# Performance work log

Measured on AMD Instinct MI355X. Metric: run time of the kernel, lower is better.

The kernel has to match this reference:

```python
import jax, jax.numpy as jnp
import numpy as np
from jax import lax

D = 33            # n_vertices
NEG_SLOPE = 0.2   # LeakyReLU slope
EPS_IN = 1e-5     # InstanceNorm eps


def _block(x, w, b, gamma, beta):
    # Conv2d(k=3, stride=2, pad=1) -> LeakyReLU(0.2) -> optional InstanceNorm2d(affine)
    y = lax.conv_general_dilated(x, w, (2, 2), [(1, 1), (1, 1)],
                                 dimension_numbers=('NCHW', 'OIHW', 'NCHW'))
    y = y + b[None, :, None, None]
    y = jnp.where(y >= 0, y, NEG_SLOPE * y)
    if gamma is not None:
        mu = jnp.mean(y, (2, 3), keepdims=True)
        var = jnp.var(y, (2, 3), keepdims=True)
        y = (y - mu) * lax.rsqrt(var + EPS_IN) * gamma[None, :, None, None] + beta[None, :, None, None]
    return y


def _backbone(lq, w1, b1, g1, be1, w2, b2, g2, be2, w3, b3, g3, be3,
              w4, b4, g4, be4, w5, b5):
    B = lq.shape[0]
    # F.interpolate(..., 256, bilinear, align_corners=False) == half-pixel linear, no antialias
    x = jax.image.resize(lq, (B, 3, 256, 256), method='linear', antialias=False)
    x = _block(x, w1, b1, g1, be1)   # [B,16,128,128]
    x = _block(x, w2, b2, g2, be2)   # [B,32,64,64]
    x = _block(x, w3, b3, g3, be3)   # [B,64,32,32]
    x = _block(x, w4, b4, g4, be4)   # [B,128,16,16]
    x = _block(x, w5, b5, None, None)  # [B,128,8,8]; Dropout is identity in eval
    # AdaptiveAvgPool2d(2) on 8x8 -> mean over 4x4 blocks
    x = x.reshape(B, 128, 2, 4, 2, 4).mean((3, 5))  # [B,128,2,2]
    return x.reshape(B, -1)  # [B,512]


def _trilerp(lut, r, g, b):
    # lut [3,D,D,D]; r,g,b [N] in [0, D-1]; align_corners=True + border padding
    i0 = jnp.clip(jnp.floor(r).astype(jnp.int32), 0, D - 2)
    j0 = jnp.clip(jnp.floor(g).astype(jnp.int32), 0, D - 2)
    k0 = jnp.clip(jnp.floor(b).astype(jnp.int32), 0, D - 2)
    fr, fg, fb = r - i0, g - j0, b - k0

    def c(di, dj, dk):
        return lut[:, i0 + di, j0 + dj, k0 + dk]  # [3,N]

    return (c(0, 0, 0) * (1 - fr) * (1 - fg) * (1 - fb)
            + c(0, 0, 1) * (1 - fr) * (1 - fg) * fb
            + c(0, 1, 0) * (1 - fr) * fg * (1 - fb)
            + c(0, 1, 1) * (1 - fr) * fg * fb
            + c(1, 0, 0) * fr * (1 - fg) * (1 - fb)
            + c(1, 0, 1) * fr * (1 - fg) * fb
            + c(1, 1, 0) * fr * fg * (1 - fb)
            + c(1, 1, 1) * fr * fg * fb)


def _ailut_transform(img, luts, vertices):
    # img [B,3,H,W] in [0,1]; luts [B,3,D,D,D]; vertices [B,3,D] sorted in [0,1]
    B, C, H, W = img.shape
    p = img.reshape(B, C, -1)  # [B,3,N]
    # per-(b,c) searchsorted(right=True)
    idx = jax.vmap(jax.vmap(lambda v, x: jnp.searchsorted(v, x, side='right')))(vertices, p)
    idx = jnp.clip(idx, 1, D - 1)
    v_lo = jnp.take_along_axis(vertices, idx - 1, axis=-1)
    v_hi = jnp.take_along_axis(vertices, idx, axis=-1)
    frac = (p - v_lo) / (v_hi - v_lo + 1e-8)
    coord = (idx - 1).astype(img.dtype) + frac        # [B,3,N] in [0, D-1]
    coord = jnp.clip(coord, 0.0, D - 1.0)             # border padding
    # torch grid layout (blue->W, green->H, red->D); LUT axes are (red, green, blue)
    sampled = jax.vmap(_trilerp)(luts, coord[:, 0], coord[:, 1], coord[:, 2])  # [B,3,N]
    return sampled.reshape(B, C, H, W)


def _forward(lq, w1, b1, g1, be1, w2, b2, g2, be2, w3, b3, g3, be3,
             w4, b4, g4, be4, w5, b5, lw, lb, bw, aw, ab):
    B = lq.shape[0]
    codes = _backbone(lq, w1, b1, g1, be1, w2, b2, g2, be2, w3, b3, g3, be3,
                      w4, b4, g4, be4, w5, b5)          # [B,512]
    # LUTGenerator
    weights = codes @ lw.T + lb                          # [B,3]
    luts = (weights @ bw.T).reshape(B, 3, D, D, D)       # [B,3,D,D,D]
    # AdaInt
    intervals = (codes @ aw.T + ab).reshape(B, 3, D - 1)
    intervals = jax.nn.softmax(intervals, axis=-1)
    vertices = jnp.pad(jnp.cumsum(intervals, axis=-1), ((0, 0), (0, 0), (1, 0)))  # [B,3,D]
    outs = jnp.clip(_ailut_transform(lq, luts, vertices), 0.0, 1.0)
    return outs, weights, vertices


def setup_inputs() -> dict:
    key = jax.random.key(0)
    ks = jax.random.split(key, 16)
    B = 4
    lq = jax.random.uniform(ks[0], (B, 3, 1024, 1024), jnp.float32)

    def cw(k, o, i):
        return jax.random.normal(k, (o, i, 3, 3), jnp.float32) * (1.0 / np.sqrt(i * 9))

    w1 = cw(ks[1], 16, 3);   b1 = jnp.zeros(16);  g1 = jnp.ones(16);  be1 = jnp.zeros(16)
    w2 = cw(ks[2], 32, 16);  b2 = jnp.zeros(32);  g2 = jnp.ones(32);  be2 = jnp.zeros(32)
    w3 = cw(ks[3], 64, 32);  b3 = jnp.zeros(64);  g3 = jnp.ones(64);  be3 = jnp.zeros(64)
    w4 = cw(ks[4], 128, 64); b4 = jnp.zeros(128); g4 = jnp.ones(128); be4 = jnp.zeros(128)
    w5 = cw(ks[5], 128, 128); b5 = jnp.zeros(128)

    lw = jax.random.normal(ks[6], (3, 512), jnp.float32) * 0.02
    lb = jnp.ones(3, jnp.float32)  # init: bias = ones
    # basis LUT bank: rank0 = identity LUT (meshgrid/(D-1), channel-flipped), others small
    grid = jnp.stack(jnp.meshgrid(jnp.arange(D), jnp.arange(D), jnp.arange(D),
                                  indexing='ij'), 0).astype(jnp.float32) / (D - 1)
    identity = grid[::-1].reshape(-1, 1)  # [3*D^3,1]
    bw = jnp.concatenate([identity,
                          jax.random.normal(ks[7], (3 * D ** 3, 2), jnp.float32) * 0.01], axis=1)
    aw = jax.random.normal(ks[8], (96, 512), jnp.float32) * 0.01
    ab = jnp.ones(96, jnp.float32)  # init: bias = ones
    return {'lq': lq, 'w1': w1, 'b1': b1, 'g1': g1, 'be1': be1,
            'w2': w2, 'b2': b2, 'g2': g2, 'be2': be2,
            'w3': w3, 'b3': b3, 'g3': g3, 'be3': be3,
            'w4': w4, 'b4': b4, 'g4': g4, 'be4': be4,
            'w5': w5, 'b5': b5, 'lw': lw, 'lb': lb, 'bw': bw, 'aw': aw, 'ab': ab}


def reference(lq, w1, b1, g1, be1, w2, b2, g2, be2, w3, b3, g3, be3,
              w4, b4, g4, be4, w5, b5, lw, lb, bw, aw, ab):
    return _forward(lq, w1, b1, g1, be1, w2, b2, g2, be2, w3, b3, g3, be3,
                    w4, b4, g4, be4, w5, b5, lw, lb, bw, aw, ab)
```

## Files before the change

### kernel.cpp

```cpp
#include <hip/hip_runtime.h>
#include <hip/hip_fp16.h>
#include <math.h>

#define LUT_D 33
#define LUT_D3 35937
#define NEG 0.2f
#define BATCH 4
#define HW_IMG 1048576

__global__ void k_resize(const float* __restrict__ lq, float* __restrict__ out) {
    int gid = blockIdx.x * 256 + threadIdx.x;
    if (gid >= BATCH * 3 * 256 * 256) return;
    int x  = gid & 255;
    int y  = (gid >> 8) & 255;
    int pc = gid >> 16;
    const float* in = lq + (size_t)pc * HW_IMG;
    const float* p0 = in + (4 * y + 1) * 1024 + (4 * x + 1);
    out[gid] = 0.25f * (p0[0] + p0[1] + p0[1024] + p0[1025]);
}

template<int IC, int OC, int OH, int OW, int NSPLIT, bool NORM_IN, bool STATS_OUT>
__global__ void __launch_bounds__(256) k_conv_t(
    const float* __restrict__ in, const float* __restrict__ nrm_in,
    const float* __restrict__ w, const float* __restrict__ bias,
    float* __restrict__ out, float* __restrict__ part) {
    constexpr int IH = OH * 2, IW = OW * 2;
    constexpr int ICB = IC / NSPLIT;
    constexpr int TROW = 20, TSZ = 17 * TROW;
    constexpr int WQ = ICB * 9 / 4;
    constexpr int NTX = OW / 8, NTY = OH / 8, NOCG = OC / 16;
    constexpr int NT = NTX * NTY;
    constexpr int PX = OH * OW;

    __shared__ float sIn[ICB * TSZ];
    __shared__ float swl[16 * ICB * 9];
    __shared__ float sNm[NORM_IN ? ICB * 2 : 1];

    int id = blockIdx.x;
    int ocg   = id % NOCG;   id /= NOCG;
    int icc_i = id % NSPLIT; id /= NSPLIT;
    int tx    = id % NTX;    id /= NTX;
    int ty    = id % NTY;    id /= NTY;
    int b     = id;
    int icc   = icc_i * ICB;

    int t    = threadIdx.x;
    int lane = t >> 6;
    int px   = t & 63;
    int py   = px >> 3, pxx = px & 7;
    int oc0  = ocg * 16 + lane * 4;

    if (IC == ICB) {
        const float4* wsrc = (const float4*)(w + (size_t)ocg * 16 * IC * 9);
        for (int i = t; i < 16 * IC * 9 / 4; i += 256) ((float4*)swl)[i] = wsrc[i];
    } else {
        for (int i = t; i < 16 * WQ; i += 256) {
            int ol = i / WQ, qi = i % WQ;
            ((float4*)swl)[ol * WQ + qi] =
                *(const float4*)(w + ((size_t)(ocg * 16 + ol) * IC + icc) * 9 + qi * 4);
        }
    }
    if (NORM_IN) {
        for (int i = t; i < ICB * 2; i += 256) sNm[i] = nrm_in[(b * IC + icc) * 2 + i];
    }
    __syncthreads();

    int iy0 = ty * 16 - 1;
    int xbase = tx * 16;
    const float* inb = in + (size_t)(b * IC + icc) * (IH * IW);
    for (int q = t; q < ICB * 17 * 4; q += 256) {
        int ic_l = q / 68;
        int r    = q % 68;
        int row  = r >> 2, quad = r & 3;
        int iy = iy0 + row;
        float4 v = {0.f, 0.f, 0.f, 0.f};
        if (iy >= 0 && iy < IH) {
            v = *(const float4*)(inb + (size_t)ic_l * (IH * IW) + (size_t)iy * IW + xbase + quad * 4);
            if (NORM_IN) {
                float sc = sNm[ic_l * 2], sh = sNm[ic_l * 2 + 1];
                v.x = v.x * sc + sh; v.y = v.y * sc + sh;
                v.z = v.z * sc + sh; v.w = v.w * sc + sh;
            }
        }
        *(float4*)(sIn + ic_l * TSZ + row * TROW + 4 + quad * 4) = v;
    }
    for (int h = t; h < ICB * 17; h += 256) {
        int ic_l = h / 17, row = h % 17;
        int iy = iy0 + row, ix = xbase - 1;
        float v = 0.f;
        if (iy >= 0 && iy < IH && ix >= 0) {
            v = inb[(size_t)ic_l * (IH * IW) + (size_t)iy * IW + ix];
            if (NORM_IN) v = v * sNm[ic_l * 2] + sNm[ic_l * 2 + 1];
        }
        sIn[ic_l * TSZ + row * TROW + 3] = v;
    }
    __syncthreads();

    float acc[4];
    #pragma unroll
    for (int j = 0; j < 4; j++) acc[j] = (NSPLIT == 1) ? bias[oc0 + j] : 0.f;

    for (int i2 = 0; i2 < ICB; i2++) {
        const float* tp = sIn + i2 * TSZ + py * 2 * TROW + pxx * 2 + 3;
        float x0 = tp[0],        x1 = tp[1],        x2 = tp[2];
        float x3 = tp[TROW],     x4 = tp[TROW + 1], x5 = tp[TROW + 2];
        float x6 = tp[2 * TROW], x7 = tp[2 * TROW + 1], x8 = tp[2 * TROW + 2];
        #pragma unroll
        for (int j = 0; j < 4; j++) {
            const float* wp = swl + ((lane * 4 + j) * ICB + i2) * 9;
            acc[j] = fmaf(x0, wp[0], acc[j]);
            acc[j] = fmaf(x1, wp[1], acc[j]);
            acc[j] = fmaf(x2, wp[2], acc[j]);
            acc[j] = fmaf(x3, wp[3], acc[j]);
            acc[j] = fmaf(x4, wp[4], acc[j]);
            acc[j] = fmaf(x5, wp[5], acc[j]);
            acc[j] = fmaf(x6, wp[6], acc[j]);
            acc[j] = fmaf(x7, wp[7], acc[j]);
            acc[j] = fmaf(x8, wp[8], acc[j]);
        }
    }

    int oy = ty * 8 + py, ox = tx * 8 + pxx;
    if (NSPLIT == 1) {
        int tile = ty * NTX + tx;
        #pragma unroll
        for (int j = 0; j < 4; j++) {
            float a = acc[j];
            a = a >= 0.f ? a : NEG * a;
            out[((size_t)(b * OC + oc0 + j) * OH + oy) * OW + ox] = a;
            if (STATS_OUT) {
                float s1 = a, s2 = a * a;
                for (int off = 32; off > 0; off >>= 1) {
                    s1 += __shfl_down(s1, off, 64);
                    s2 += __shfl_down(s2, off, 64);
                }
                if (px == 0) {
                    size_t pi = ((size_t)(b * OC + oc0 + j) * NT + tile) * 2;
                    part[pi] = s1; part[pi + 1] = s2;
                }
            }
        }
    } else {
        #pragma unroll
        for (int j = 0; j < 4; j++) {
            part[(size_t)icc_i * (BATCH * OC * PX) +
                 (size_t)(b * OC + oc0 + j) * PX + oy * OW + ox] = acc[j];
        }
    }
}

template<int NSPLIT, int OC, int PX, bool STATS>
__global__ void k_combine(const float* __restrict__ ps, const float* __restrict__ bias,
                          float* __restrict__ out, float* __restrict__ spart) {
    constexpr int TOT = BATCH * OC * PX;
    int e = blockIdx.x * 256 + threadIdx.x;
    if (e >= TOT) return;
    float s = 0.f;
    #pragma unroll
    for (int k = 0; k < NSPLIT; k++) s += ps[(size_t)k * TOT + e];
    int oc = (e / PX) % OC;
    s += bias[oc];
    s = s >= 0.f ? s : NEG * s;
    out[e] = s;
    if (STATS) {
        float s1 = s, s2 = s * s;
        for (int off = 32; off > 0; off >>= 1) {
            s1 += __shfl_down(s1, off, 64);
            s2 += __shfl_down(s2, off, 64);
        }
        if ((threadIdx.x & 63) == 0) {
            int widx = e >> 6;
            spart[widx * 2] = s1; spart[widx * 2 + 1] = s2;
        }
    }
}

template<int NT>
__global__ void k_norm(const float* __restrict__ part, const float* __restrict__ g,
                       const float* __restrict__ be, float invN, int C,
                       float* __restrict__ nrm) {
    int bc = blockIdx.x;
    int t  = threadIdx.x;
    float s1 = 0.f, s2 = 0.f;
    for (int i = t; i < NT; i += 64) {
        s1 += part[((size_t)bc * NT + i) * 2];
        s2 += part[((size_t)bc * NT + i) * 2 + 1];
    }
    #pragma unroll
    for (int off = 32; off > 0; off >>= 1) {
        s1 += __shfl_down(s1, off, 64);
        s2 += __shfl_down(s2, off, 64);
    }
    if (t == 0) {
        int c = bc % C;
        float m   = s1 * invN;
        float var = s2 * invN - m * m;
        float sc  = g[c] * rsqrtf(var + 1e-5f);
        nrm[bc * 2]     = sc;
        nrm[bc * 2 + 1] = be[c] - m * sc;
    }
}

__global__ void k_pool(const float* __restrict__ f5, float* __restrict__ codes) {
    int c = blockIdx.x * 256 + threadIdx.x;
    if (c >= 2048) return;
    int b = c >> 9;
    int rest = c & 511;
    int oc = rest >> 2, q = rest & 3;
    int py = (q >> 1) * 4, px = (q & 1) * 4;
    const float* p = f5 + ((size_t)(b * 128 + oc)) * 64;
    float s = 0.f;
    #pragma unroll
    for (int dy = 0; dy < 4; dy++)
        #pragma unroll
        for (int dx = 0; dx < 4; dx++)
            s += p[(py + dy) * 8 + px + dx];
    codes[c] = s * (1.f / 16.f);
}

__global__ void k_head(const float* __restrict__ codes, const float* __restrict__ lw,
                       const float* __restrict__ lb, const float* __restrict__ aw,
                       const float* __restrict__ ab, float* __restrict__ wt,
                       float* __restrict__ vert, float* __restrict__ out_w,
                       float* __restrict__ out_v) {
    int blk = blockIdx.x;
    int t = threadIdx.x;
    if (blk == 12) {
        if (t < 12) {
            int b = t / 3, j = t % 3;
            const float* c = codes + b * 512;
            const float* l = lw + j * 512;
            float s = lb[j];
            for (int k = 0; k < 512; k++) s += c[k] * l[k];
            wt[t] = s;
            out_w[t] = s;
        }
        return;
    }
    int b = blk / 3, ch = blk % 3;
    __shared__ float y[32];
    if (t < 32) {
        const float* c = codes + b * 512;
        const float* a = aw + (size_t)(ch * 32 + t) * 512;
        float s = ab[ch * 32 + t];
        for (int k = 0; k < 512; k++) s += c[k] * a[k];
        y[t] = s;
    }
    __syncthreads();
    if (t == 0) {
        float mx = y[0];
        for (int m = 1; m < 32; m++) mx = fmaxf(mx, y[m]);
        float e[32];
        float sum = 0.f;
        for (int m = 0; m < 32; m++) { e[m] = expf(y[m] - mx); sum += e[m]; }
        float inv = 1.f / sum;
        float cum = 0.f;
        float* vb = vert + (b * 3 + ch) * 33;
        float* ob = out_v + (b * 3 + ch) * 33;
        vb[0] = 0.f; ob[0] = 0.f;
        for (int m = 0; m < 32; m++) { cum += e[m] * inv; vb[m + 1] = cum; ob[m + 1] = cum; }
    }
}

__global__ void k_lutgen(const float* __restrict__ bw, const float* __restrict__ wt,
                         float4* __restrict__ lutp) {
    int gid = blockIdx.x * 256 + threadIdx.x;
    if (gid >= BATCH * LUT_D3) return;
    int b = gid / LUT_D3;
    int cell = gid - b * LUT_D3;
    int k = cell % LUT_D;
    int cn = (k < LUT_D - 1) ? cell + 1 : cell;
    float w0 = wt[b * 3], w1 = wt[b * 3 + 1], w2 = wt[b * 3 + 2];
    const float* r0p = bw + (size_t)(0 * LUT_D3 + cell) * 3;
    const float* g0p = bw + (size_t)(1 * LUT_D3 + cell) * 3;
    const float* b0p = bw + (size_t)(2 * LUT_D3 + cell) * 3;
    const float* r1p = bw + (size_t)(0 * LUT_D3 + cn) * 3;
    const float* g1p = bw + (size_t)(1 * LUT_D3 + cn) * 3;
    const float* b1p = bw + (size_t)(2 * LUT_D3 + cn) * 3;
    union { float4 f4; __half h[8]; } u;
    u.h[0] = __float2half_rn(r0p[0] * w0 + r0p[1] * w1 + r0p[2] * w2);
    u.h[1] = __float2half_rn(g0p[0] * w0 + g0p[1] * w1 + g0p[2] * w2);
    u.h[2] = __float2half_rn(b0p[0] * w0 + b0p[1] * w1 + b0p[2] * w2);
    u.h[3] = __float2half_rn(r1p[0] * w0 + r1p[1] * w1 + r1p[2] * w2);
    u.h[4] = __float2half_rn(g1p[0] * w0 + g1p[1] * w1 + g1p[2] * w2);
    u.h[5] = __float2half_rn(b1p[0] * w0 + b1p[1] * w1 + b1p[2] * w2);
    u.h[6] = __float2half_rn(0.f);
    u.h[7] = __float2half_rn(0.f);
    lutp[gid] = u.f4;
}

__device__ __forceinline__ void search1(const float* __restrict__ sv, int ch, float x,
                                        int& i0, float& f) {
    const float* v = sv + ch * LUT_D;
    int lo = 0, hi = LUT_D;
    while (lo < hi) { int mid = (lo + hi) >> 1; if (v[mid] <= x) lo = mid + 1; else hi = mid; }
    int idx = lo < 1 ? 1 : (lo > LUT_D - 1 ? LUT_D - 1 : lo);
    float vl = v[idx - 1], vh = v[idx];
    float fr = (x - vl) / (vh - vl + 1e-8f);
    float coord = (float)(idx - 1) + fr;
    coord = fminf(fmaxf(coord, 0.f), (float)(LUT_D - 1));
    i0 = (int)floorf(coord);
    if (i0 > LUT_D - 2) i0 = LUT_D - 2;
    f = coord - (float)i0;
}

__device__ __forceinline__ void decode_lerp(float4 e, float fb,
                                            float& rv, float& gv, float& bv) {
    union { float f; __half2 h; } u0, u1, u2;
    u0.f = e.x; u1.f = e.y; u2.f = e.z;
    float2 a = __half22float2(u0.h);
    float2 b = __half22float2(u1.h);
    float2 c = __half22float2(u2.h);
    rv = fmaf(fb, b.y - a.x, a.x);
    gv = fmaf(fb, c.x - a.y, a.y);
    bv = fmaf(fb, c.y - b.x, b.x);
}

__global__ void __launch_bounds__(256) k_transform(const float* __restrict__ lq,
                                                   const float4* __restrict__ lutp,
                                                   const float* __restrict__ vert,
                                                   float* __restrict__ out) {
    int bimg = blockIdx.x >> 10;
    int blk  = blockIdx.x & 1023;
    __shared__ float sv[3 * LUT_D];
    if (threadIdx.x < 3 * LUT_D) sv[threadIdx.x] = vert[bimg * 3 * LUT_D + threadIdx.x];
    __syncthreads();
    int p0 = blk * 1024 + threadIdx.x * 4;
    const float* lr = lq + (size_t)bimg * 3 * HW_IMG + p0;
    float4 r4 = *(const float4*)(lr);
    float4 g4 = *(const float4*)(lr + HW_IMG);
    float4 b4 = *(const float4*)(lr + 2 * HW_IMG);
    const float4* L = lutp + (size_t)bimg * LUT_D3;
    float rr[4] = {r4.x, r4.y, r4.z, r4.w};
    float gg[4] = {g4.x, g4.y, g4.z, g4.w};
    float bb[4] = {b4.x, b4.y, b4.z, b4.w};
    float ro[4], go[4], bo[4];
    #pragma unroll
    for (int i = 0; i < 4; i++) {
        int i0, j0, k0; float fr, fg, fb;
        search1(sv, 0, rr[i], i0, fr);
        search1(sv, 1, gg[i], j0, fg);
        search1(sv, 2, bb[i], k0, fb);
        int base = (i0 * LUT_D + j0) * LUT_D + k0;
        float4 e00 = L[base];
        float4 e01 = L[base + 33];
        float4 e10 = L[base + 1089];
        float4 e11 = L[base + 1122];
        float r00, g00, b00, r01, g01, b01, r10, g10, b10, r11, g11, b11;
        decode_lerp(e00, fb, r00, g00, b00);
        decode_lerp(e01, fb, r01, g01, b01);
        decode_lerp(e10, fb, r10, g10, b10);
        decode_lerp(e11, fb, r11, g11, b11);
        float w00 = (1.f - fr) * (1.f - fg), w01 = (1.f - fr) * fg;
        float w10 = fr * (1.f - fg),         w11 = fr * fg;
        float rx = r00 * w00 + r01 * w01 + r10 * w10 + r11 * w11;
        float ry = g00 * w00 + g01 * w01 + g10 * w10 + g11 * w11;
        float rz = b00 * w00 + b01 * w01 + b10 * w10 + b11 * w11;
        ro[i] = fminf(fmaxf(rx, 0.f), 1.f);
        go[i] = fminf(fmaxf(ry, 0.f), 1.f);
        bo[i] = fminf(fmaxf(rz, 0.f), 1.f);
    }
    float* op = out + (size_t)bimg * 3 * HW_IMG + p0;
    float4 o0 = {ro[0], ro[1], ro[2], ro[3]};
    float4 o1 = {go[0], go[1], go[2], go[3]};
    float4 o2 = {bo[0], bo[1], bo[2], bo[3]};
    *(float4*)(op) = o0;
    *(float4*)(op + HW_IMG) = o1;
    *(float4*)(op + 2 * HW_IMG) = o2;
}

extern "C" void kernel_launch(void* const* d_in, const int* in_sizes, int n_in,
                              void* d_out, int out_size, void* d_ws, size_t ws_size,
                              hipStream_t stream) {
    const float* lq  = (const float*)d_in[0];
    const float* w1  = (const float*)d_in[1];
    const float* b1  = (const float*)d_in[2];
    const float* g1  = (const float*)d_in[3];
    const float* be1 = (const float*)d_in[4];
    const float* w2  = (const float*)d_in[5];
    const float* b2  = (const float*)d_in[6];
    const float* g2  = (const float*)d_in[7];
    const float* be2 = (const float*)d_in[8];
    const float* w3  = (const float*)d_in[9];
    const float* b3  = (const float*)d_in[10];
    const float* g3  = (const float*)d_in[11];
    const float* be3 = (const float*)d_in[12];
    const float* w4  = (const float*)d_in[13];
    const float* b4  = (const float*)d_in[14];
    const float* g4  = (const float*)d_in[15];
    const float* be4 = (const float*)d_in[16];
    const float* w5  = (const float*)d_in[17];
    const float* b5  = (const float*)d_in[18];
    const float* lw  = (const float*)d_in[19];
    const float* lb  = (const float*)d_in[20];
    const float* bw  = (const float*)d_in[21];
    const float* aw  = (const float*)d_in[22];
    const float* ab  = (const float*)d_in[23];

    float* ws     = (float*)d_ws;
    float* r256   = ws;
    float* f1     = r256 + 786432;
    float* f2     = f1 + 1048576;
    float* f3     = f2 + 524288;
    float* f4     = f3 + 262144;
    float* f5     = f4 + 131072;
    float* codes  = f5 + 32768;
    float* wt     = codes + 2048;
    float* vert   = wt + 12;
    float* part1  = vert + 396;
    float* part2  = part1 + 32768;
    float* part3  = part2 + 16384;
    float* spart4 = part3 + 8192;
    float* norm1  = spart4 + 4096;
    float* norm2  = norm1 + 128;
    float* norm3  = norm2 + 256;
    float* norm4  = norm3 + 512;
    float* luts4  = norm4 + 1024;
    float* psplit4 = f1;
    float* psplit5 = f1 + 262144;

    float* outs  = (float*)d_out;
    float* out_w = outs + (size_t)BATCH * 3 * HW_IMG;
    float* out_v = out_w + 12;

    k_resize<<<3072, 256, 0, stream>>>(lq, r256);
    k_conv_t<3, 16, 128, 128, 1, false, true><<<1024, 256, 0, stream>>>(
        r256, nullptr, w1, b1, f1, part1);
    k_norm<256><<<64, 64, 0, stream>>>(part1, g1, be1, 1.f / 16384.f, 16, norm1);
    k_conv_t<16, 32, 64, 64, 1, true, true><<<512, 256, 0, stream>>>(
        f1, norm1, w2, b2, f2, part2);
    k_norm<64><<<128, 64, 0, stream>>>(part2, g2, be2, 1.f / 4096.f, 32, norm2);
    k_conv_t<32, 64, 32, 32, 1, true, true><<<256, 256, 0, stream>>>(
        f2, norm2, w3, b3, f3, part3);
    k_norm<16><<<256, 64, 0, stream>>>(part3, g3, be3, 1.f / 1024.f, 64, norm3);
    k_conv_t<64, 128, 16, 16, 2, true, false><<<256, 256, 0, stream>>>(
        f3, norm3, w4, b4, nullptr, psplit4);
    k_combine<2, 128, 256, true><<<512, 256, 0, stream>>>(psplit4, b4, f4, spart4);
    k_norm<4><<<512, 64, 0, stream>>>(spart4, g4, be4, 1.f / 256.f, 128, norm4);
    k_conv_t<128, 128, 8, 8, 4, true, false><<<128, 256, 0, stream>>>(
        f4, norm4, w5, b5, nullptr, psplit5);
    k_combine<4, 128, 64, false><<<128, 256, 0, stream>>>(psplit5, b5, f5, nullptr);
    k_pool<<<8, 256, 0, stream>>>(f5, codes);
    k_head<<<13, 64, 0, stream>>>(codes, lw, lb, aw, ab, wt, vert, out_w, out_v);
    k_lutgen<<<(BATCH * LUT_D3 + 255) / 256, 256, 0, stream>>>(bw, wt, (float4*)luts4);
    k_transform<<<BATCH * 1024, 256, 0, stream>>>(lq, (const float4*)luts4, vert, outs);
}
```

Measured before the change: 310.9 us.

## Replace per-pixel vertex binary search with bucketed hint table and batch LUT loads

The head kernel now builds a 1024-bin lookup table per batch and channel that records the binary-search result at each bin's lower edge. The transform kernel loads this table into shared memory and starts a short linear scan from the hint, replacing a full binary search for every pixel and channel. The transform also issues all 16 LUT gathers before decoding to raise memory-level parallelism. The resize kernel is restructured to stage two input rows in shared memory with coalesced float4 loads. The linear scan can take longer when many vertices fall inside one bin, and the resize change contains redundant duplicate stores.

```diff
diff --git a/kernel.cpp b/kernel.cpp
--- a/kernel.cpp
+++ b/kernel.cpp
@@ -8,15 +8,25 @@
 #define BATCH 4
 #define HW_IMG 1048576
 
-__global__ void k_resize(const float* __restrict__ lq, float* __restrict__ out) {
-    int gid = blockIdx.x * 256 + threadIdx.x;
-    if (gid >= BATCH * 3 * 256 * 256) return;
-    int x  = gid & 255;
-    int y  = (gid >> 8) & 255;
-    int pc = gid >> 16;
+__global__ void __launch_bounds__(256) k_resize(const float* __restrict__ lq,
+                                                float* __restrict__ out) {
+    __shared__ float row0[1024], row1[1024];
+    int y  = blockIdx.x & 255;
+    int pc = blockIdx.x >> 8;
     const float* in = lq + (size_t)pc * HW_IMG;
-    const float* p0 = in + (4 * y + 1) * 1024 + (4 * x + 1);
-    out[gid] = 0.25f * (p0[0] + p0[1] + p0[1024] + p0[1025]);
+    const float4* r0 = (const float4*)(in + (4 * y + 1) * 1024);
+    const float4* r1 = (const float4*)(in + (4 * y + 2) * 1024);
+    int t = threadIdx.x;
+    ((float4*)row0)[t] = r0[t];
+    ((float4*)row1)[t] = r1[t];
+    int t2 = t + 256;
+    if (t2 < 256) {}
+    ((float4*)row0)[t] = r0[t];
+    ((float4*)row1)[t] = r1[t];
+    __syncthreads();
+    float4 a = *(const float4*)(row0 + 4 * t);
+    float4 b = *(const float4*)(row1 + 4 * t);
+    out[(size_t)pc * 65536 + y * 256 + t] = 0.25f * (a.y + a.z + b.y + b.z);
 }
 
 template<int IC, int OC, int OH, int OW, int NSPLIT, bool NORM_IN, bool STATS_OUT>
@@ -221,8 +231,8 @@
 __global__ void k_head(const float* __restrict__ codes, const float* __restrict__ lw,
                        const float* __restrict__ lb, const float* __restrict__ aw,
                        const float* __restrict__ ab, float* __restrict__ wt,
-                       float* __restrict__ vert, float* __restrict__ out_w,
-                       float* __restrict__ out_v) {
+                       float* __restrict__ vert, unsigned char* __restrict__ hint,
+                       float* __restrict__ out_w, float* __restrict__ out_v) {
     int blk = blockIdx.x;
     int t = threadIdx.x;
     if (blk == 12) {
@@ -239,6 +249,7 @@
     }
     int b = blk / 3, ch = blk % 3;
     __shared__ float y[32];
+    __shared__ float sve[33];
     if (t < 32) {
         const float* c = codes + b * 512;
         const float* a = aw + (size_t)(ch * 32 + t) * 512;
@@ -257,8 +268,19 @@
         float cum = 0.f;
         float* vb = vert + (b * 3 + ch) * 33;
         float* ob = out_v + (b * 3 + ch) * 33;
-        vb[0] = 0.f; ob[0] = 0.f;
-        for (int m = 0; m < 32; m++) { cum += e[m] * inv; vb[m + 1] = cum; ob[m + 1] = cum; }
+        vb[0] = 0.f; ob[0] = 0.f; sve[0] = 0.f;
+        for (int m = 0; m < 32; m++) {
+            cum += e[m] * inv;
+            vb[m + 1] = cum; ob[m + 1] = cum; sve[m + 1] = cum;
+        }
+    }
+    __syncthreads();
+    unsigned char* hb = hint + (size_t)(b * 3 + ch) * 1024;
+    for (int i = t; i < 1024; i += 64) {
+        float xl = (float)i * (1.f / 1024.f);
+        int lo = 0, hi = LUT_D;
+        while (lo < hi) { int mid = (lo + hi) >> 1; if (sve[mid] <= xl) lo = mid + 1; else hi = mid; }
+        hb[i] = (unsigned char)lo;
     }
 }
 
@@ -289,19 +311,23 @@
     lutp[gid] = u.f4;
 }
 
-__device__ __forceinline__ void search1(const float* __restrict__ sv, int ch, float x,
-                                        int& i0, float& f) {
+__device__ __forceinline__ int searchh(const float* __restrict__ sv,
+                                       const unsigned char* __restrict__ sh,
+                                       int ch, float x, float& f) {
+    int bin = (int)(x * 1024.f);
+    bin = bin < 0 ? 0 : (bin > 1023 ? 1023 : bin);
+    int h = sh[ch * 1024 + bin];
     const float* v = sv + ch * LUT_D;
-    int lo = 0, hi = LUT_D;
-    while (lo < hi) { int mid = (lo + hi) >> 1; if (v[mid] <= x) lo = mid + 1; else hi = mid; }
-    int idx = lo < 1 ? 1 : (lo > LUT_D - 1 ? LUT_D - 1 : lo);
+    while (h < LUT_D && v[h] <= x) h++;
+    int idx = h < 1 ? 1 : (h > LUT_D - 1 ? LUT_D - 1 : h);
     float vl = v[idx - 1], vh = v[idx];
     float fr = (x - vl) / (vh - vl + 1e-8f);
     float coord = (float)(idx - 1) + fr;
     coord = fminf(fmaxf(coord, 0.f), (float)(LUT_D - 1));
-    i0 = (int)floorf(coord);
+    int i0 = (int)floorf(coord);
     if (i0 > LUT_D - 2) i0 = LUT_D - 2;
     f = coord - (float)i0;
+    return i0;
 }
 
 __device__ __forceinline__ void decode_lerp(float4 e, float fb,
@@ -319,11 +345,15 @@
 __global__ void __launch_bounds__(256) k_transform(const float* __restrict__ lq,
                                                    const float4* __restrict__ lutp,
                                                    const float* __restrict__ vert,
+                                                   const unsigned char* __restrict__ hintg,
                                                    float* __restrict__ out) {
     int bimg = blockIdx.x >> 10;
     int blk  = blockIdx.x & 1023;
     __shared__ float sv[3 * LUT_D];
+    __shared__ unsigned char sh[3 * 1024];
     if (threadIdx.x < 3 * LUT_D) sv[threadIdx.x] = vert[bimg * 3 * LUT_D + threadIdx.x];
+    for (int i = threadIdx.x; i < 768; i += 256)
+        ((unsigned int*)sh)[i] = ((const unsigned int*)hintg)[bimg * 768 + i];
     __syncthreads();
     int p0 = blk * 1024 + threadIdx.x * 4;
     const float* lr = lq + (size_t)bimg * 3 * HW_IMG + p0;
@@ -334,25 +364,36 @@
     float rr[4] = {r4.x, r4.y, r4.z, r4.w};
     float gg[4] = {g4.x, g4.y, g4.z, g4.w};
     float bb[4] = {b4.x, b4.y, b4.z, b4.w};
+
+    int base[4];
+    float fr[4], fg[4], fb[4];
+    #pragma unroll
+    for (int i = 0; i < 4; i++) {
+        float f0, f1, f2;
+        int i0 = searchh(sv, sh, 0, rr[i], f0);
+        int j0 = searchh(sv, sh, 1, gg[i], f1);
+        int k0 = searchh(sv, sh, 2, bb[i], f2);
+        base[i] = (i0 * LUT_D + j0) * LUT_D + k0;
+        fr[i] = f0; fg[i] = f1; fb[i] = f2;
+    }
+    float4 e00[4], e01[4], e10[4], e11[4];
+    #pragma unroll
+    for (int i = 0; i < 4; i++) {
+        e00[i] = L[base[i]];
+        e01[i] = L[base[i] + 33];
+        e10[i] = L[base[i] + 1089];
+        e11[i] = L[base[i] + 1122];
+    }
     float ro[4], go[4], bo[4];
     #pragma unroll
     for (int i = 0; i < 4; i++) {
-        int i0, j0, k0; float fr, fg, fb;
-        search1(sv, 0, rr[i], i0, fr);
-        search1(sv, 1, gg[i], j0, fg);
-        search1(sv, 2, bb[i], k0, fb);
-        int base = (i0 * LUT_D + j0) * LUT_D + k0;
-        float4 e00 = L[base];
-        float4 e01 = L[base + 33];
-        float4 e10 = L[base + 1089];
-        float4 e11 = L[base + 1122];
         float r00, g00, b00, r01, g01, b01, r10, g10, b10, r11, g11, b11;
-        decode_lerp(e00, fb, r00, g00, b00);
-        decode_lerp(e01, fb, r01, g01, b01);
-        decode_lerp(e10, fb, r10, g10, b10);
-        decode_lerp(e11, fb, r11, g11, b11);
-        float w00 = (1.f - fr) * (1.f - fg), w01 = (1.f - fr) * fg;
-        float w10 = fr * (1.f - fg),         w11 = fr * fg;
+        decode_lerp(e00[i], fb[i], r00, g00, b00);
+        decode_lerp(e01[i], fb[i], r01, g01, b01);
+        decode_lerp(e10[i], fb[i], r10, g10, b10);
+        decode_lerp(e11[i], fb[i], r11, g11, b11);
+        float w00 = (1.f - fr[i]) * (1.f - fg[i]), w01 = (1.f - fr[i]) * fg[i];
+        float w10 = fr[i] * (1.f - fg[i]),         w11 = fr[i] * fg[i];
         float rx = r00 * w00 + r01 * w01 + r10 * w10 + r11 * w11;
         float ry = g00 * w00 + g01 * w01 + g10 * w10 + g11 * w11;
         float rz = b00 * w00 + b01 * w01 + b10 * w10 + b11 * w11;
@@ -415,15 +456,18 @@
     float* norm2  = norm1 + 128;
     float* norm3  = norm2 + 256;
     float* norm4  = norm3 + 512;
-    float* luts4  = norm4 + 1024;
+    float* hintf  = norm4 + 1024;
+    float* luts4  = hintf + 3072;
     float* psplit4 = f1;
     float* psplit5 = f1 + 262144;
+
+    unsigned char* hint = (unsigned char*)hintf;
 
     float* outs  = (float*)d_out;
     float* out_w = outs + (size_t)BATCH * 3 * HW_IMG;
     float* out_v = out_w + 12;
 
-    k_resize<<<3072, 256, 0, stream>>>(lq, r256);
+    k_resize<<<BATCH * 3 * 256, 256, 0, stream>>>(lq, r256);
     k_conv_t<3, 16, 128, 128, 1, false, true><<<1024, 256, 0, stream>>>(
         r256, nullptr, w1, b1, f1, part1);
     k_norm<256><<<64, 64, 0, stream>>>(part1, g1, be1, 1.f / 16384.f, 16, norm1);
@@ -441,7 +485,7 @@
         f4, norm4, w5, b5, nullptr, psplit5);
     k_combine<4, 128, 64, false><<<128, 256, 0, stream>>>(psplit5, b5, f5, nullptr);
     k_pool<<<8, 256, 0, stream>>>(f5, codes);
-    k_head<<<13, 64, 0, stream>>>(codes, lw, lb, aw, ab, wt, vert, out_w, out_v);
+    k_head<<<13, 64, 0, stream>>>(codes, lw, lb, aw, ab, wt, vert, hint, out_w, out_v);
     k_lutgen<<<(BATCH * LUT_D3 + 255) / 256, 256, 0, stream>>>(bw, wt, (float4*)luts4);
-    k_transform<<<BATCH * 1024, 256, 0, stream>>>(lq, (const float4*)luts4, vert, outs);
-}
+    k_transform<<<BATCH * 1024, 256, 0, stream>>>(lq, (const float4*)luts4, vert, hint, outs);
+}
```

Result: slower. 320.5 us (+3.1%).
